# Kernel optimization log

Hardware: AMD Instinct MI355X
Metric: run time of the kernel (lower is better)

## Reference

```python
import jax, jax.numpy as jnp
import numpy as np

K = 10
ALPHA = 0.1
N_NODES = 100000
N_EDGES = 1600000
IN_DIM = 128
HID_DIM = 128
OUT_DIM = 128


def setup_inputs() -> dict:
    key = jax.random.key(0)
    k_x, k_e, k_w1, k_b1, k_w2, k_b2 = jax.random.split(key, 6)
    x = jax.random.normal(k_x, (N_NODES, IN_DIM), dtype=jnp.float32)
    edge_index = jax.random.randint(k_e, (2, N_EDGES), 0, N_NODES, dtype=jnp.int64)
    # Linear params (Kaiming-uniform-ish scale, exact init irrelevant for correctness)
    s1 = 1.0 / np.sqrt(IN_DIM)
    s2 = 1.0 / np.sqrt(HID_DIM)
    W1 = jax.random.uniform(k_w1, (IN_DIM, HID_DIM), jnp.float32, -s1, s1)
    b1 = jax.random.uniform(k_b1, (HID_DIM,), jnp.float32, -s1, s1)
    W2 = jax.random.uniform(k_w2, (HID_DIM, OUT_DIM), jnp.float32, -s2, s2)
    b2 = jax.random.uniform(k_b2, (OUT_DIM,), jnp.float32, -s2, s2)
    return {"x": x, "edge_index": edge_index, "W1": W1, "b1": b1, "W2": W2, "b2": b2}


def reference(x, edge_index, W1, b1, W2, b2):
    n = x.shape[0]
    h = jax.nn.relu(x @ W1 + b1)  # [N, H]

    # gcn_norm: add self loops, symmetric normalization D^-1/2 (A+I) D^-1/2
    loop = jnp.arange(n, dtype=edge_index.dtype)
    src = jnp.concatenate([edge_index[0], loop])  # [E+N]
    dst = jnp.concatenate([edge_index[1], loop])  # [E+N]
    ones = jnp.ones(src.shape[0], dtype=h.dtype)
    deg = jax.ops.segment_sum(ones, dst, num_segments=n)  # [N]
    dinv = jnp.where(deg > 0, jax.lax.rsqrt(deg), 0.0)
    norm = (dinv[src] * dinv[dst])[:, None]  # [E+N, 1]

    # APPNP: K steps of h = (1-alpha) * A_hat h + alpha * h0
    h0 = h

    def step(h, _):
        msg = norm * h[src]  # gather + scale  [E+N, H]
        agg = jax.ops.segment_sum(msg, dst, num_segments=n)  # scatter-add [N, H]
        return (1.0 - ALPHA) * agg + ALPHA * h0, None

    h, _ = jax.lax.scan(step, h, None, length=K)
    return h @ W2 + b2
```

## Files before the change

kernel.cpp:

```cpp
#include <hip/hip_runtime.h>
#include <stdint.h>

#define N_NODES 100000
#define N_EDGES 1600000
#define HDIM    128
#define KSTEPS  10
#define NZONE   8
#define ZDIV    12500u

typedef unsigned int uint;

#define SCAN_T     256
#define SCAN_I     4
#define SCAN_ELEMS (SCAN_T * SCAN_I)
#define SCAN_NB    ((N_NODES + SCAN_ELEMS - 1) / SCAN_ELEMS)

__device__ inline float2 bf2_to_f2(uint v) {
    float2 r;
    r.x = __uint_as_float(v << 16);
    r.y = __uint_as_float(v & 0xffff0000u);
    return r;
}
__device__ inline uint f_to_bf_bits(float f) {
    uint u = __float_as_uint(f);
    return (u + 0x7fffu + ((u >> 16) & 1u)) >> 16;
}
__device__ inline uint f2_to_bf2(float x, float y) {
    return f_to_bf_bits(x) | (f_to_bf_bits(y) << 16);
}

__global__ void k_countpos(const int* __restrict__ eidx, int* __restrict__ cnt,
                           int* __restrict__ pos) {
    int e0 = (blockIdx.x * blockDim.x + threadIdx.x) * 4;
    if (e0 < N_EDGES) {
        int4 d4 = *(const int4*)&eidx[N_EDGES + e0];
        int4 p;
        p.x = atomicAdd(&cnt[d4.x], 1);
        p.y = atomicAdd(&cnt[d4.y], 1);
        p.z = atomicAdd(&cnt[d4.z], 1);
        p.w = atomicAdd(&cnt[d4.w], 1);
        *(int4*)&pos[e0] = p;
    }
}

__global__ void k_scan1(const int* __restrict__ cnt, int* __restrict__ rp,
                        int* __restrict__ bsum) {
    __shared__ int s[SCAN_T];
    int tid  = threadIdx.x;
    int base = blockIdx.x * SCAN_ELEMS + tid * SCAN_I;
    int v[SCAN_I];
    int loc = 0;
#pragma unroll
    for (int j = 0; j < SCAN_I; ++j) {
        int idx = base + j;
        v[j] = (idx < N_NODES) ? cnt[idx] : 0;
        loc += v[j];
    }
    s[tid] = loc;
    __syncthreads();
    for (int off = 1; off < SCAN_T; off <<= 1) {
        int t = (tid >= off) ? s[tid - off] : 0;
        __syncthreads();
        s[tid] += t;
        __syncthreads();
    }
    int run = s[tid] - loc;
#pragma unroll
    for (int j = 0; j < SCAN_I; ++j) {
        int idx = base + j;
        if (idx < N_NODES) rp[idx] = run;
        run += v[j];
    }
    if (tid == SCAN_T - 1) bsum[blockIdx.x] = s[SCAN_T - 1];
}

__global__ void k_scan2(const int* __restrict__ bsum, int* __restrict__ boff,
                        int* __restrict__ rp) {
    int acc = 0;
    for (int i = 0; i < SCAN_NB; ++i) { boff[i] = acc; acc += bsum[i]; }
    rp[N_NODES] = acc;
}

__global__ void k_scan3(int* __restrict__ rp, const int* __restrict__ boff) {
    int off = boff[blockIdx.x];
#pragma unroll
    for (int j = 0; j < SCAN_I; ++j) {
        int i = blockIdx.x * SCAN_ELEMS + threadIdx.x + j * SCAN_T;
        if (i < N_NODES) rp[i] += off;
    }
}

__global__ void k_dinv(const int* __restrict__ cnt, float* __restrict__ dinv,
                       float* __restrict__ dsq) {
    int i = blockIdx.x * blockDim.x + threadIdx.x;
    if (i < N_NODES) {
        float d = 1.0f + (float)cnt[i];
        dinv[i] = rsqrtf(d);
        dsq[i]  = sqrtf(d);
    }
}

#define FCHUNK 8192
#define FECH   ((N_EDGES + FCHUNK - 1) / FCHUNK)
__global__ __launch_bounds__(256)
void k_fill2(const int* __restrict__ eidx, const int* __restrict__ rp,
             const int* __restrict__ pos, int* __restrict__ col) {
    uint zone = blockIdx.x;
    int  base = blockIdx.y * FCHUNK;
#pragma unroll
    for (int i = 0; i < FCHUNK / 1024; ++i) {
        int e0 = base + (i * 256 + (int)threadIdx.x) * 4;
        if (e0 < N_EDGES) {
            int4 d4 = *(const int4*)&eidx[N_EDGES + e0];
            int4 s4 = *(const int4*)&eidx[e0];
            int4 p4 = *(const int4*)&pos[e0];
            if ((uint)d4.x / ZDIV == zone) col[rp[d4.x] + p4.x] = s4.x;
            if ((uint)d4.y / ZDIV == zone) col[rp[d4.y] + p4.y] = s4.y;
            if ((uint)d4.z / ZDIV == zone) col[rp[d4.z] + p4.z] = s4.z;
            if ((uint)d4.w / ZDIV == zone) col[rp[d4.w] + p4.w] = s4.w;
        }
    }
}

#define KCH 64
__global__ __launch_bounds__(256)
void k_gemm1(const float* __restrict__ x, const float* __restrict__ W,
             const float* __restrict__ bias, const float* __restrict__ dinv,
             uint* __restrict__ out) {
    __shared__ __align__(16) float wlds[KCH][HDIM];
    __shared__ __align__(16) float xs[32][KCH + 1];
    int tid  = threadIdx.x;
    int tx   = tid & 31, ty = tid >> 5;
    int row0 = blockIdx.x * 32;

    float4 bc = *(const float4*)&bias[tx * 4];

    float acc[4][4] = {};
    for (int kc = 0; kc < HDIM; kc += KCH) {
#pragma unroll
        for (int i = 0; i < 8; ++i) {
            int id = tid + i * 256;
            int kk = id >> 5, n4 = id & 31;
            *(float4*)&wlds[kk][n4 * 4] =
                *(const float4*)&W[(size_t)(kc + kk) * HDIM + n4 * 4];
        }
#pragma unroll
        for (int i = 0; i < 2; ++i) {
            int id = tid + i * 256;
            int r = id >> 4, c4 = id & 15;
            float4 v = *(const float4*)&x[(size_t)(row0 + r) * HDIM + kc + c4 * 4];
            xs[r][c4 * 4 + 0] = v.x;
            xs[r][c4 * 4 + 1] = v.y;
            xs[r][c4 * 4 + 2] = v.z;
            xs[r][c4 * 4 + 3] = v.w;
        }
        __syncthreads();
#pragma unroll 8
        for (int kk = 0; kk < KCH; ++kk) {
            float4 b4 = *(const float4*)&wlds[kk][tx * 4];
            float a0 = xs[ty * 4 + 0][kk];
            float a1 = xs[ty * 4 + 1][kk];
            float a2 = xs[ty * 4 + 2][kk];
            float a3 = xs[ty * 4 + 3][kk];
            acc[0][0] += a0 * b4.x; acc[0][1] += a0 * b4.y; acc[0][2] += a0 * b4.z; acc[0][3] += a0 * b4.w;
            acc[1][0] += a1 * b4.x; acc[1][1] += a1 * b4.y; acc[1][2] += a1 * b4.z; acc[1][3] += a1 * b4.w;
            acc[2][0] += a2 * b4.x; acc[2][1] += a2 * b4.y; acc[2][2] += a2 * b4.z; acc[2][3] += a2 * b4.w;
            acc[3][0] += a3 * b4.x; acc[3][1] += a3 * b4.y; acc[3][2] += a3 * b4.z; acc[3][3] += a3 * b4.w;
        }
        __syncthreads();
    }
#pragma unroll
    for (int r = 0; r < 4; ++r) {
        int row = row0 + ty * 4 + r;
        float di = dinv[row];
        float v0 = fmaxf(acc[r][0] + bc.x, 0.0f) * di;
        float v1 = fmaxf(acc[r][1] + bc.y, 0.0f) * di;
        float v2 = fmaxf(acc[r][2] + bc.z, 0.0f) * di;
        float v3 = fmaxf(acc[r][3] + bc.w, 0.0f) * di;
        uint2 p;
        p.x = f2_to_bf2(v0, v1);
        p.y = f2_to_bf2(v2, v3);
        *(uint2*)&out[(size_t)row * 64 + tx * 2] = p;
    }
}

__global__ __launch_bounds__(256)
void k_gemm2(const uint* __restrict__ u, const float* __restrict__ W,
             const float* __restrict__ bias, const float* __restrict__ dsq,
             float* __restrict__ out) {
    __shared__ __align__(16) float wlds[KCH][HDIM];
    __shared__ __align__(16) float xs[32][KCH + 1];
    int tid  = threadIdx.x;
    int tx   = tid & 31, ty = tid >> 5;
    int row0 = blockIdx.x * 32;

    float4 bc = *(const float4*)&bias[tx * 4];

    float acc[4][4] = {};
    for (int kc = 0; kc < HDIM; kc += KCH) {
#pragma unroll
        for (int i = 0; i < 8; ++i) {
            int id = tid + i * 256;
            int kk = id >> 5, n4 = id & 31;
            *(float4*)&wlds[kk][n4 * 4] =
                *(const float4*)&W[(size_t)(kc + kk) * HDIM + n4 * 4];
        }
#pragma unroll
        for (int i = 0; i < 2; ++i) {
            int id = tid + i * 256;
            int r = id >> 4, c4 = id & 15;
            float ds = dsq[row0 + r];
            uint2 v = *(const uint2*)&u[(size_t)(row0 + r) * 64 + (kc >> 1) + c4 * 2];
            float2 f0 = bf2_to_f2(v.x);
            float2 f1 = bf2_to_f2(v.y);
            xs[r][c4 * 4 + 0] = f0.x * ds;
            xs[r][c4 * 4 + 1] = f0.y * ds;
            xs[r][c4 * 4 + 2] = f1.x * ds;
            xs[r][c4 * 4 + 3] = f1.y * ds;
        }
        __syncthreads();
#pragma unroll 8
        for (int kk = 0; kk < KCH; ++kk) {
            float4 b4 = *(const float4*)&wlds[kk][tx * 4];
            float a0 = xs[ty * 4 + 0][kk];
            float a1 = xs[ty * 4 + 1][kk];
            float a2 = xs[ty * 4 + 2][kk];
            float a3 = xs[ty * 4 + 3][kk];
            acc[0][0] += a0 * b4.x; acc[0][1] += a0 * b4.y; acc[0][2] += a0 * b4.z; acc[0][3] += a0 * b4.w;
            acc[1][0] += a1 * b4.x; acc[1][1] += a1 * b4.y; acc[1][2] += a1 * b4.z; acc[1][3] += a1 * b4.w;
            acc[2][0] += a2 * b4.x; acc[2][1] += a2 * b4.y; acc[2][2] += a2 * b4.z; acc[2][3] += a2 * b4.w;
            acc[3][0] += a3 * b4.x; acc[3][1] += a3 * b4.y; acc[3][2] += a3 * b4.z; acc[3][3] += a3 * b4.w;
        }
        __syncthreads();
    }
#pragma unroll
    for (int r = 0; r < 4; ++r) {
        int row = row0 + ty * 4 + r;
        float4 v;
        v.x = acc[r][0] + bc.x;
        v.y = acc[r][1] + bc.y;
        v.z = acc[r][2] + bc.z;
        v.w = acc[r][3] + bc.w;
        *(float4*)&out[(size_t)row * HDIM + tx * 4] = v;
    }
}

__global__ __launch_bounds__(256)
void k_step(const uint* __restrict__ uin, const uint* __restrict__ u0,
            uint* __restrict__ uout, const int* __restrict__ col,
            const int* __restrict__ rp, const float* __restrict__ dinv) {
    int wid  = (blockIdx.x * blockDim.x + threadIdx.x) >> 6;
    int node = __builtin_amdgcn_readfirstlane(wid);
    int lane = threadIdx.x & 63;
    if (node >= N_NODES) return;

    size_t self = (size_t)node * 64 + lane;
    uint usv = uin[self];
    uint uzv = __builtin_nontemporal_load(&u0[self]);
    float di = dinv[node];
    float w  = 0.9f * di * di;

    int beg = rp[node], end = rp[node + 1];
    float2 us = bf2_to_f2(usv);
    float accx = us.x, accy = us.y;

    int e = beg;
    for (; e + 8 <= end; e += 8) {
        int s0 = col[e + 0], s1 = col[e + 1], s2 = col[e + 2], s3 = col[e + 3];
        int s4 = col[e + 4], s5 = col[e + 5], s6 = col[e + 6], s7 = col[e + 7];
        uint b0 = uin[(size_t)s0 * 64 + lane];
        uint b1 = uin[(size_t)s1 * 64 + lane];
        uint b2 = uin[(size_t)s2 * 64 + lane];
        uint b3 = uin[(size_t)s3 * 64 + lane];
        uint b4 = uin[(size_t)s4 * 64 + lane];
        uint b5 = uin[(size_t)s5 * 64 + lane];
        uint b6 = uin[(size_t)s6 * 64 + lane];
        uint b7 = uin[(size_t)s7 * 64 + lane];
        float2 a0 = bf2_to_f2(b0), a1 = bf2_to_f2(b1);
        float2 a2 = bf2_to_f2(b2), a3 = bf2_to_f2(b3);
        float2 a4 = bf2_to_f2(b4), a5 = bf2_to_f2(b5);
        float2 a6 = bf2_to_f2(b6), a7 = bf2_to_f2(b7);
        accx += ((a0.x + a1.x) + (a2.x + a3.x)) + ((a4.x + a5.x) + (a6.x + a7.x));
        accy += ((a0.y + a1.y) + (a2.y + a3.y)) + ((a4.y + a5.y) + (a6.y + a7.y));
    }
    if (e + 4 <= end) {
        int s0 = col[e], s1 = col[e + 1], s2 = col[e + 2], s3 = col[e + 3];
        uint b0 = uin[(size_t)s0 * 64 + lane];
        uint b1 = uin[(size_t)s1 * 64 + lane];
        uint b2 = uin[(size_t)s2 * 64 + lane];
        uint b3 = uin[(size_t)s3 * 64 + lane];
        float2 a0 = bf2_to_f2(b0), a1 = bf2_to_f2(b1);
        float2 a2 = bf2_to_f2(b2), a3 = bf2_to_f2(b3);
        accx += (a0.x + a1.x) + (a2.x + a3.x);
        accy += (a0.y + a1.y) + (a2.y + a3.y);
        e += 4;
    }
    if (e + 2 <= end) {
        int s0 = col[e], s1 = col[e + 1];
        uint b0 = uin[(size_t)s0 * 64 + lane];
        uint b1 = uin[(size_t)s1 * 64 + lane];
        float2 a0 = bf2_to_f2(b0), a1 = bf2_to_f2(b1);
        accx += a0.x + a1.x;
        accy += a0.y + a1.y;
        e += 2;
    }
    if (e < end) {
        uint b0 = uin[(size_t)col[e] * 64 + lane];
        float2 a0 = bf2_to_f2(b0);
        accx += a0.x;
        accy += a0.y;
    }
    float2 uz = bf2_to_f2(uzv);
    float ox = w * accx + 0.1f * uz.x;
    float oy = w * accy + 0.1f * uz.y;
    __builtin_nontemporal_store(f2_to_bf2(ox, oy), &uout[self]);
}

extern "C" void kernel_launch(void* const* d_in, const int* in_sizes, int n_in,
                              void* d_out, int out_size, void* d_ws, size_t ws_size,
                              hipStream_t stream) {
    (void)in_sizes; (void)n_in; (void)out_size; (void)ws_size;
    const float* x  = (const float*)d_in[0];
    const int*   ei = (const int*)d_in[1];
    const float* W1 = (const float*)d_in[2];
    const float* b1 = (const float*)d_in[3];
    const float* W2 = (const float*)d_in[4];
    const float* b2 = (const float*)d_in[5];
    float* out = (float*)d_out;

    char* ws = (char*)d_ws;
    size_t off = 0;
    auto alloc = [&](size_t bytes) -> void* {
        void* p = ws + off;
        off += (bytes + 255) & ~(size_t)255;
        return p;
    };
    uint*  u0   = (uint*)alloc(sizeof(uint) * (size_t)N_NODES * 64);
    uint*  uA   = (uint*)alloc(sizeof(uint) * (size_t)N_NODES * 64);
    uint*  uB   = (uint*)alloc(sizeof(uint) * (size_t)N_NODES * 64);
    int*   col  = (int*)alloc(sizeof(int) * N_EDGES);
    int*   pos  = (int*)alloc(sizeof(int) * N_EDGES);
    int*   rp   = (int*)alloc(sizeof(int) * (N_NODES + 1));
    int*   cnt  = (int*)alloc(sizeof(int) * N_NODES);
    float* dinv = (float*)alloc(sizeof(float) * N_NODES);
    float* dsq  = (float*)alloc(sizeof(float) * N_NODES);
    int*   bsum = (int*)alloc(sizeof(int) * SCAN_NB);
    int*   boff = (int*)alloc(sizeof(int) * SCAN_NB);

    hipMemsetAsync(cnt, 0, sizeof(int) * N_NODES, stream);

    k_countpos<<<(N_EDGES / 4 + 255) / 256, 256, 0, stream>>>(ei, cnt, pos);
    k_scan1<<<SCAN_NB, SCAN_T, 0, stream>>>(cnt, rp, bsum);
    k_scan2<<<1, 1, 0, stream>>>(bsum, boff, rp);
    k_scan3<<<SCAN_NB, SCAN_T, 0, stream>>>(rp, boff);
    k_dinv<<<(N_NODES + 255) / 256, 256, 0, stream>>>(cnt, dinv, dsq);
    {
        dim3 g(NZONE, FECH);
        k_fill2<<<g, 256, 0, stream>>>(ei, rp, pos, col);
    }

    k_gemm1<<<N_NODES / 32, 256, 0, stream>>>(x, W1, b1, dinv, u0);

    const uint* uin = u0;
    uint* uout = uA;
    for (int k = 0; k < KSTEPS; ++k) {
        k_step<<<N_NODES / 4, 256, 0, stream>>>(uin, u0, uout, col, rp, dinv);
        uin = uout;
        uout = (uout == uA) ? uB : uA;
    }
    k_gemm2<<<N_NODES / 32, 256, 0, stream>>>(uin, W2, b2, dsq, out);
}
```

Baseline: 924.9 us.

## Fuse APPNP propagation steps into one cooperative kernel with grid sync; use fp16

Replaces the ten per-step propagation kernel launches with a single cooperative kernel of 1024 blocks that loops over the steps and uses a grid-wide barrier between them, with each block handling a fixed contiguous node range. This removes per-launch overhead and launch gaps. The intermediate storage also changes from bf16 to fp16 packing, which gives more mantissa precision but a narrower range. In exchange, the fixed partition of nodes to blocks can create load imbalance and tail waits at each barrier, and the final output buffer is hardcoded to uB, which is correct only because KSTEPS is even.

```diff
diff --git a/kernel.cpp b/kernel.cpp
--- a/kernel.cpp
+++ b/kernel.cpp
@@ -1,5 +1,9 @@
 #include <hip/hip_runtime.h>
+#include <hip/hip_fp16.h>
+#include <hip/hip_cooperative_groups.h>
 #include <stdint.h>
+
+namespace cg = cooperative_groups;
 
 #define N_NODES 100000
 #define N_EDGES 1600000
@@ -7,6 +11,8 @@
 #define KSTEPS  10
 #define NZONE   8
 #define ZDIV    12500u
+#define PBLK    1024
+#define NPB     ((N_NODES + PBLK - 1) / PBLK)
 
 typedef unsigned int uint;
 
@@ -15,18 +21,13 @@
 #define SCAN_ELEMS (SCAN_T * SCAN_I)
 #define SCAN_NB    ((N_NODES + SCAN_ELEMS - 1) / SCAN_ELEMS)
 
-__device__ inline float2 bf2_to_f2(uint v) {
-    float2 r;
-    r.x = __uint_as_float(v << 16);
-    r.y = __uint_as_float(v & 0xffff0000u);
-    return r;
-}
-__device__ inline uint f_to_bf_bits(float f) {
-    uint u = __float_as_uint(f);
-    return (u + 0x7fffu + ((u >> 16) & 1u)) >> 16;
-}
-__device__ inline uint f2_to_bf2(float x, float y) {
-    return f_to_bf_bits(x) | (f_to_bf_bits(y) << 16);
+__device__ inline float2 h2_to_f2(uint v) {
+    __half2 h = *reinterpret_cast<__half2*>(&v);
+    return __half22float2(h);
+}
+__device__ inline uint f2_to_h2(float x, float y) {
+    __half2 h = __floats2half2_rn(x, y);
+    return *reinterpret_cast<uint*>(&h);
 }
 
 __global__ void k_countpos(const int* __restrict__ eidx, int* __restrict__ cnt,
@@ -178,8 +179,8 @@
         float v2 = fmaxf(acc[r][2] + bc.z, 0.0f) * di;
         float v3 = fmaxf(acc[r][3] + bc.w, 0.0f) * di;
         uint2 p;
-        p.x = f2_to_bf2(v0, v1);
-        p.y = f2_to_bf2(v2, v3);
+        p.x = f2_to_h2(v0, v1);
+        p.y = f2_to_h2(v2, v3);
         *(uint2*)&out[(size_t)row * 64 + tx * 2] = p;
     }
 }
@@ -211,8 +212,8 @@
             int r = id >> 4, c4 = id & 15;
             float ds = dsq[row0 + r];
             uint2 v = *(const uint2*)&u[(size_t)(row0 + r) * 64 + (kc >> 1) + c4 * 2];
-            float2 f0 = bf2_to_f2(v.x);
-            float2 f1 = bf2_to_f2(v.y);
+            float2 f0 = h2_to_f2(v.x);
+            float2 f1 = h2_to_f2(v.y);
             xs[r][c4 * 4 + 0] = f0.x * ds;
             xs[r][c4 * 4 + 1] = f0.y * ds;
             xs[r][c4 * 4 + 2] = f1.x * ds;
@@ -246,74 +247,85 @@
 }
 
 __global__ __launch_bounds__(256)
-void k_step(const uint* __restrict__ uin, const uint* __restrict__ u0,
-            uint* __restrict__ uout, const int* __restrict__ col,
-            const int* __restrict__ rp, const float* __restrict__ dinv) {
-    int wid  = (blockIdx.x * blockDim.x + threadIdx.x) >> 6;
-    int node = __builtin_amdgcn_readfirstlane(wid);
+void k_appnp(const uint* __restrict__ u0, uint* __restrict__ uA,
+             uint* __restrict__ uB, const int* __restrict__ col,
+             const int* __restrict__ rp, const float* __restrict__ dinv) {
+    cg::grid_group grid = cg::this_grid();
+    int wave = threadIdx.x >> 6;
     int lane = threadIdx.x & 63;
-    if (node >= N_NODES) return;
-
-    size_t self = (size_t)node * 64 + lane;
-    uint usv = uin[self];
-    uint uzv = __builtin_nontemporal_load(&u0[self]);
-    float di = dinv[node];
-    float w  = 0.9f * di * di;
-
-    int beg = rp[node], end = rp[node + 1];
-    float2 us = bf2_to_f2(usv);
-    float accx = us.x, accy = us.y;
-
-    int e = beg;
-    for (; e + 8 <= end; e += 8) {
-        int s0 = col[e + 0], s1 = col[e + 1], s2 = col[e + 2], s3 = col[e + 3];
-        int s4 = col[e + 4], s5 = col[e + 5], s6 = col[e + 6], s7 = col[e + 7];
-        uint b0 = uin[(size_t)s0 * 64 + lane];
-        uint b1 = uin[(size_t)s1 * 64 + lane];
-        uint b2 = uin[(size_t)s2 * 64 + lane];
-        uint b3 = uin[(size_t)s3 * 64 + lane];
-        uint b4 = uin[(size_t)s4 * 64 + lane];
-        uint b5 = uin[(size_t)s5 * 64 + lane];
-        uint b6 = uin[(size_t)s6 * 64 + lane];
-        uint b7 = uin[(size_t)s7 * 64 + lane];
-        float2 a0 = bf2_to_f2(b0), a1 = bf2_to_f2(b1);
-        float2 a2 = bf2_to_f2(b2), a3 = bf2_to_f2(b3);
-        float2 a4 = bf2_to_f2(b4), a5 = bf2_to_f2(b5);
-        float2 a6 = bf2_to_f2(b6), a7 = bf2_to_f2(b7);
-        accx += ((a0.x + a1.x) + (a2.x + a3.x)) + ((a4.x + a5.x) + (a6.x + a7.x));
-        accy += ((a0.y + a1.y) + (a2.y + a3.y)) + ((a4.y + a5.y) + (a6.y + a7.y));
-    }
-    if (e + 4 <= end) {
-        int s0 = col[e], s1 = col[e + 1], s2 = col[e + 2], s3 = col[e + 3];
-        uint b0 = uin[(size_t)s0 * 64 + lane];
-        uint b1 = uin[(size_t)s1 * 64 + lane];
-        uint b2 = uin[(size_t)s2 * 64 + lane];
-        uint b3 = uin[(size_t)s3 * 64 + lane];
-        float2 a0 = bf2_to_f2(b0), a1 = bf2_to_f2(b1);
-        float2 a2 = bf2_to_f2(b2), a3 = bf2_to_f2(b3);
-        accx += (a0.x + a1.x) + (a2.x + a3.x);
-        accy += (a0.y + a1.y) + (a2.y + a3.y);
-        e += 4;
-    }
-    if (e + 2 <= end) {
-        int s0 = col[e], s1 = col[e + 1];
-        uint b0 = uin[(size_t)s0 * 64 + lane];
-        uint b1 = uin[(size_t)s1 * 64 + lane];
-        float2 a0 = bf2_to_f2(b0), a1 = bf2_to_f2(b1);
-        accx += a0.x + a1.x;
-        accy += a0.y + a1.y;
-        e += 2;
-    }
-    if (e < end) {
-        uint b0 = uin[(size_t)col[e] * 64 + lane];
-        float2 a0 = bf2_to_f2(b0);
-        accx += a0.x;
-        accy += a0.y;
-    }
-    float2 uz = bf2_to_f2(uzv);
-    float ox = w * accx + 0.1f * uz.x;
-    float oy = w * accy + 0.1f * uz.y;
-    __builtin_nontemporal_store(f2_to_bf2(ox, oy), &uout[self]);
+    int nbeg = blockIdx.x * NPB;
+    int nend = nbeg + NPB;
+    if (nend > N_NODES) nend = N_NODES;
+
+    const uint* uin = u0;
+    uint* uout = uA;
+    for (int k = 0; k < KSTEPS; ++k) {
+        for (int node = nbeg + wave; node < nend; node += 4) {
+            size_t self = (size_t)node * 64 + lane;
+            uint usv = uin[self];
+            uint uzv = __builtin_nontemporal_load(&u0[self]);
+            float di = dinv[node];
+            float w  = 0.9f * di * di;
+
+            int beg = rp[node], end = rp[node + 1];
+            float2 us = h2_to_f2(usv);
+            float accx = us.x, accy = us.y;
+
+            int e = beg;
+            for (; e + 8 <= end; e += 8) {
+                int s0 = col[e + 0], s1 = col[e + 1], s2 = col[e + 2], s3 = col[e + 3];
+                int s4 = col[e + 4], s5 = col[e + 5], s6 = col[e + 6], s7 = col[e + 7];
+                uint b0 = uin[(size_t)s0 * 64 + lane];
+                uint b1 = uin[(size_t)s1 * 64 + lane];
+                uint b2 = uin[(size_t)s2 * 64 + lane];
+                uint b3 = uin[(size_t)s3 * 64 + lane];
+                uint b4 = uin[(size_t)s4 * 64 + lane];
+                uint b5 = uin[(size_t)s5 * 64 + lane];
+                uint b6 = uin[(size_t)s6 * 64 + lane];
+                uint b7 = uin[(size_t)s7 * 64 + lane];
+                float2 a0 = h2_to_f2(b0), a1 = h2_to_f2(b1);
+                float2 a2 = h2_to_f2(b2), a3 = h2_to_f2(b3);
+                float2 a4 = h2_to_f2(b4), a5 = h2_to_f2(b5);
+                float2 a6 = h2_to_f2(b6), a7 = h2_to_f2(b7);
+                accx += ((a0.x + a1.x) + (a2.x + a3.x)) + ((a4.x + a5.x) + (a6.x + a7.x));
+                accy += ((a0.y + a1.y) + (a2.y + a3.y)) + ((a4.y + a5.y) + (a6.y + a7.y));
+            }
+            if (e + 4 <= end) {
+                int s0 = col[e], s1 = col[e + 1], s2 = col[e + 2], s3 = col[e + 3];
+                uint b0 = uin[(size_t)s0 * 64 + lane];
+                uint b1 = uin[(size_t)s1 * 64 + lane];
+                uint b2 = uin[(size_t)s2 * 64 + lane];
+                uint b3 = uin[(size_t)s3 * 64 + lane];
+                float2 a0 = h2_to_f2(b0), a1 = h2_to_f2(b1);
+                float2 a2 = h2_to_f2(b2), a3 = h2_to_f2(b3);
+                accx += (a0.x + a1.x) + (a2.x + a3.x);
+                accy += (a0.y + a1.y) + (a2.y + a3.y);
+                e += 4;
+            }
+            if (e + 2 <= end) {
+                int s0 = col[e], s1 = col[e + 1];
+                uint b0 = uin[(size_t)s0 * 64 + lane];
+                uint b1 = uin[(size_t)s1 * 64 + lane];
+                float2 a0 = h2_to_f2(b0), a1 = h2_to_f2(b1);
+                accx += a0.x + a1.x;
+                accy += a0.y + a1.y;
+                e += 2;
+            }
+            if (e < end) {
+                uint b0 = uin[(size_t)col[e] * 64 + lane];
+                float2 a0 = h2_to_f2(b0);
+                accx += a0.x;
+                accy += a0.y;
+            }
+            float2 uz = h2_to_f2(uzv);
+            float ox = w * accx + 0.1f * uz.x;
+            float oy = w * accy + 0.1f * uz.y;
+            uout[self] = f2_to_h2(ox, oy);
+        }
+        grid.sync();
+        uin  = uout;
+        uout = (uout == uA) ? uB : uA;
+    }
 }
 
 extern "C" void kernel_launch(void* const* d_in, const int* in_sizes, int n_in,
@@ -361,12 +373,12 @@
 
     k_gemm1<<<N_NODES / 32, 256, 0, stream>>>(x, W1, b1, dinv, u0);
 
-    const uint* uin = u0;
-    uint* uout = uA;
-    for (int k = 0; k < KSTEPS; ++k) {
-        k_step<<<N_NODES / 4, 256, 0, stream>>>(uin, u0, uout, col, rp, dinv);
-        uin = uout;
-        uout = (uout == uA) ? uB : uA;
-    }
-    k_gemm2<<<N_NODES / 32, 256, 0, stream>>>(uin, W2, b2, dsq, out);
-}
+    {
+        void* args[] = {(void*)&u0, (void*)&uA, (void*)&uB,
+                        (void*)&col, (void*)&rp, (void*)&dinv};
+        hipLaunchCooperativeKernel((void*)k_appnp, dim3(PBLK), dim3(256),
+                                   args, 0, stream);
+    }
+
+    k_gemm2<<<N_NODES / 32, 256, 0, stream>>>(uB, W2, b2, dsq, out);
+}
```

Measured after the change: 2.459 ms. 166% more time.
